# Kernel tuning notes

Measured on AMD Instinct MI355X. Metric: run time of the kernel, lower is better.

The kernel has to match this reference:

```python
import jax, jax.numpy as jnp
import numpy as np
from jax import lax

D = 512
K = 5
HID = 2 * D
EPS = 1e-5


def layernorm(x, g, b):
    mu = jnp.mean(x, axis=-1, keepdims=True)
    var = jnp.mean((x - mu) ** 2, axis=-1, keepdims=True)
    return (x - mu) * lax.rsqrt(var + EPS) * g + b


def setup_inputs() -> dict:
    key = jax.random.key(0)
    ks = jax.random.split(key, 16)
    B, T = 8, 4096
    sc = lambda fan: 1.0 / np.sqrt(fan)
    return {
        "x": jax.random.normal(ks[0], (B, T, D), jnp.float32),
        "decay_logit": jnp.zeros((D,), jnp.float32),
        "W_out": jax.random.uniform(ks[1], (D, D), jnp.float32, -sc(D), sc(D)),
        "b_out": jax.random.uniform(ks[2], (D,), jnp.float32, -sc(D), sc(D)),
        "conv_w": jax.random.uniform(ks[3], (D, 1, K), jnp.float32, -sc(K), sc(K)),
        "conv_b": jax.random.uniform(ks[4], (D,), jnp.float32, -sc(K), sc(K)),
        "ln1_g": jnp.ones((D,), jnp.float32),
        "ln1_b": jnp.zeros((D,), jnp.float32),
        "ln2_g": jnp.ones((D,), jnp.float32),
        "ln2_b": jnp.zeros((D,), jnp.float32),
        "W1": jax.random.uniform(ks[5], (HID, D), jnp.float32, -sc(D), sc(D)),
        "b1": jax.random.uniform(ks[6], (HID,), jnp.float32, -sc(D), sc(D)),
        "W2": jax.random.uniform(ks[7], (D, HID), jnp.float32, -sc(HID), sc(HID)),
        "b2": jax.random.uniform(ks[8], (D,), jnp.float32, -sc(HID), sc(HID)),
    }


def retention_core(xn, decay_logit, W_out, b_out, conv_w, conv_b):
    # xn: [B, T, D]
    B, T, _ = xn.shape
    a = jax.nn.sigmoid(decay_logit)  # [D]

    def step(s, xt):  # s, xt: [B, D]
        s = a * s + (1.0 - a) * xt
        return s, s

    s0 = jnp.zeros((B, D), xn.dtype)
    _, ss = lax.scan(step, s0, jnp.swapaxes(xn, 0, 1))  # [T, B, D]
    ss = jnp.swapaxes(ss, 0, 1)  # [B, T, D]
    y_ret = jnp.einsum("btd,ed->bte", ss, W_out) + b_out

    # depthwise conv1d, 'same' padding (K odd)
    xc = jnp.swapaxes(xn, 1, 2)  # [B, D, T]
    pad = (K - 1) // 2
    y_loc = lax.conv_general_dilated(
        xc, conv_w, window_strides=(1,), padding=[(pad, pad)],
        feature_group_count=D, dimension_numbers=("NCH", "OIH", "NCH"))
    y_loc = jnp.swapaxes(y_loc + conv_b[None, :, None], 1, 2)  # [B, T, D]
    return y_ret + y_loc


def reference(x, decay_logit, W_out, b_out, conv_w, conv_b,
              ln1_g, ln1_b, ln2_g, ln2_b, W1, b1, W2, b2):
    y = retention_core(layernorm(x, ln1_g, ln1_b),
                       decay_logit, W_out, b_out, conv_w, conv_b)
    x = x + y
    h = layernorm(x, ln2_g, ln2_b)
    h = jax.nn.gelu(jnp.einsum("btd,hd->bth", h, W1) + b1, approximate=False)
    y = jnp.einsum("bth,dh->btd", h, W2) + b2
    return x + y
```

## Files before the change

kernel.cpp:

```cpp
#include <hip/hip_runtime.h>
#include <stdint.h>

typedef unsigned short u16;

#define DIM 512
#define HIDN 1024
#define TT 4096
#define BB 8
#define MM 32768
#define CH 128
#define CL 32

__device__ __forceinline__ u16 f2bf(float f) {
  union { float f; uint32_t u; } v; v.f = f;
  uint32_t u = v.u;
  uint32_t r = u + 0x7fffu + ((u >> 16) & 1u);
  return (u16)(r >> 16);
}
__device__ __forceinline__ float bf2f(u16 h) {
  union { uint32_t u; float f; } v; v.u = ((uint32_t)h) << 16; return v.f;
}

typedef __bf16 bf16x8 __attribute__((ext_vector_type(8)));
typedef float f32x4 __attribute__((ext_vector_type(4)));

__global__ __launch_bounds__(256) void prep_kernel(
    const float* __restrict__ wout, const float* __restrict__ w1,
    const float* __restrict__ w2, const float* __restrict__ dl,
    const float* __restrict__ convw,
    u16* __restrict__ wout_h, u16* __restrict__ w1_h, u16* __restrict__ w2_h,
    float* __restrict__ a, float* __restrict__ oma, float* __restrict__ aL,
    float* __restrict__ convwT) {
  int i = blockIdx.x * 256 + threadIdx.x;
  if (i < DIM * DIM) wout_h[i] = f2bf(wout[i]);
  if (i < HIDN * DIM) { w1_h[i] = f2bf(w1[i]); w2_h[i] = f2bf(w2[i]); }
  if (i < 5 * DIM) {
    int kk = i / DIM, n = i - kk * DIM;
    convwT[i] = convw[n * 5 + kk];
  }
  if (i < DIM) {
    float av = 1.0f / (1.0f + expf(-dl[i]));
    a[i] = av; oma[i] = 1.0f - av; aL[i] = powf(av, (float)CL);
  }
}

__global__ __launch_bounds__(256) void ln_rows(
    const float* __restrict__ xin, const float* __restrict__ g,
    const float* __restrict__ bvec, u16* __restrict__ out) {
  int lane = threadIdx.x & 63, wave = threadIdx.x >> 6;
  size_t row = (size_t)blockIdx.x * 4 + wave;
  const float4* xr = (const float4*)(xin + row * DIM);
  float4 v0 = xr[lane * 2 + 0];
  float4 v1 = xr[lane * 2 + 1];
  float s1 = v0.x + v0.y + v0.z + v0.w + v1.x + v1.y + v1.z + v1.w;
  float s2 = v0.x * v0.x + v0.y * v0.y + v0.z * v0.z + v0.w * v0.w
           + v1.x * v1.x + v1.y * v1.y + v1.z * v1.z + v1.w * v1.w;
#pragma unroll
  for (int o = 1; o < 64; o <<= 1) { s1 += __shfl_xor(s1, o); s2 += __shfl_xor(s2, o); }
  float mu = s1 * (1.0f / DIM);
  float var = s2 * (1.0f / DIM) - mu * mu;
  float rs = rsqrtf(var + 1e-5f);
  const float4* gr = (const float4*)g;
  const float4* br = (const float4*)bvec;
  float4 g0 = gr[lane * 2], g1 = gr[lane * 2 + 1];
  float4 b0 = br[lane * 2], b1 = br[lane * 2 + 1];
  uint32_t p0 = (uint32_t)f2bf((v0.x - mu) * rs * g0.x + b0.x) | ((uint32_t)f2bf((v0.y - mu) * rs * g0.y + b0.y) << 16);
  uint32_t p1 = (uint32_t)f2bf((v0.z - mu) * rs * g0.z + b0.z) | ((uint32_t)f2bf((v0.w - mu) * rs * g0.w + b0.w) << 16);
  uint32_t p2 = (uint32_t)f2bf((v1.x - mu) * rs * g1.x + b1.x) | ((uint32_t)f2bf((v1.y - mu) * rs * g1.y + b1.y) << 16);
  uint32_t p3 = (uint32_t)f2bf((v1.z - mu) * rs * g1.z + b1.z) | ((uint32_t)f2bf((v1.w - mu) * rs * g1.w + b1.w) << 16);
  uint4 pk; pk.x = p0; pk.y = p1; pk.z = p2; pk.w = p3;
  ((uint4*)(out + row * DIM))[lane] = pk;
}

__global__ __launch_bounds__(256) void scan_local(
    const u16* __restrict__ xn, const float* __restrict__ a,
    const float* __restrict__ oma, float* __restrict__ carry) {
  int idx = blockIdx.x * 256 + threadIdx.x;
  int dp = (idx & 255) * 2;
  int c = (idx >> 8) & (CH - 1);
  int b = idx >> 15;
  float a0 = a[dp], a1 = a[dp + 1], o0 = oma[dp], o1 = oma[dp + 1];
  const uint32_t* xp = (const uint32_t*)(xn + ((size_t)(b * TT + c * CL)) * DIM + dp);
  float s0 = 0.f, s1 = 0.f;
#pragma unroll
  for (int i = 0; i < CL; ++i) {
    uint32_t u = xp[(size_t)i * (DIM / 2)];
    s0 = fmaf(a0, s0, o0 * bf2f((u16)(u & 0xffffu)));
    s1 = fmaf(a1, s1, o1 * bf2f((u16)(u >> 16)));
  }
  float2 cv; cv.x = s0; cv.y = s1;
  *(float2*)&carry[((size_t)(b * CH + c)) * DIM + dp] = cv;
}

__global__ __launch_bounds__(256) void scan_carry(
    const float* __restrict__ carry, const float* __restrict__ aL,
    float* __restrict__ start) {
  int idx = blockIdx.x * 256 + threadIdx.x;
  int d = idx & (DIM - 1);
  int b = idx >> 9;
  float al = aL[d];
  float s = 0.f;
#pragma unroll 8
  for (int c = 0; c < CH; ++c) {
    size_t o = ((size_t)(b * CH + c)) * DIM + d;
    start[o] = s;
    s = fmaf(al, s, carry[o]);
  }
}

__global__ __launch_bounds__(256) void scan_emit(
    const u16* __restrict__ xn, const float* __restrict__ a,
    const float* __restrict__ oma, const float* __restrict__ start,
    u16* __restrict__ ss) {
  int idx = blockIdx.x * 256 + threadIdx.x;
  int dp = (idx & 255) * 2;
  int c = (idx >> 8) & (CH - 1);
  int b = idx >> 15;
  float a0 = a[dp], a1 = a[dp + 1], o0 = oma[dp], o1 = oma[dp + 1];
  const uint32_t* xp = (const uint32_t*)(xn + ((size_t)(b * TT + c * CL)) * DIM + dp);
  uint32_t* sp = (uint32_t*)(ss + ((size_t)(b * TT + c * CL)) * DIM + dp);
  float2 st = *(const float2*)&start[((size_t)(b * CH + c)) * DIM + dp];
  float s0 = st.x, s1 = st.y;
#pragma unroll
  for (int i = 0; i < CL; ++i) {
    uint32_t u = xp[(size_t)i * (DIM / 2)];
    s0 = fmaf(a0, s0, o0 * bf2f((u16)(u & 0xffffu)));
    s1 = fmaf(a1, s1, o1 * bf2f((u16)(u >> 16)));
    sp[(size_t)i * (DIM / 2)] = (uint32_t)f2bf(s0) | ((uint32_t)f2bf(s1) << 16);
  }
}

template <int Kd, int NCOL, int EPI>
__global__ __launch_bounds__(256) void gemm_bt(
    const u16* __restrict__ A, const u16* __restrict__ Bmat,
    const float* __restrict__ bias, const float* __restrict__ resid,
    const u16* __restrict__ xn, const float* __restrict__ convwT,
    const float* __restrict__ convb, float* __restrict__ outf,
    u16* __restrict__ outh) {
  __shared__ alignas(16) u16 sA[2][128 * 64];
  __shared__ alignas(16) u16 sB[2][128 * 64];
  const int tid = threadIdx.x;
  const int lane = tid & 63, wave = tid >> 6;
  const int wr = (wave >> 1) * 64, wc = (wave & 1) * 64;
  const int rA = lane & 15, q = lane >> 4;

  const int lin = blockIdx.x;
  const int tile_col = (lin >> 3) & (NCOL - 1);
  const int tile_row = (lin & 7) + 8 * ((lin >> 3) / NCOL);
  const size_t rowTile = (size_t)tile_row * 128;
  const size_t colTile = (size_t)tile_col * 128;

  f32x4 acc[4][4];
#pragma unroll
  for (int i = 0; i < 4; i++)
#pragma unroll
    for (int j = 0; j < 4; j++) acc[i][j] = (f32x4){0.f, 0.f, 0.f, 0.f};

  const u16* Abase = A + rowTile * Kd;
  const u16* Bbase = Bmat + colTile * Kd;

  const int lrow = lane >> 3;
  const int lslot = lane & 7;
  const int gk = ((lslot ^ lrow) & 7) * 8;

  auto stage = [&](int kt, int buf) {
#pragma unroll
    for (int it = 0; it < 4; ++it) {
      const int m0 = (it * 4 + wave) * 8;
      const u16* ga = Abase + (size_t)(m0 + lrow) * Kd + kt + gk;
      const u16* gb = Bbase + (size_t)(m0 + lrow) * Kd + kt + gk;
      __builtin_amdgcn_global_load_lds(
          (const __attribute__((address_space(1))) void*)ga,
          (__attribute__((address_space(3))) void*)&sA[buf][m0 * 64], 16, 0, 0);
      __builtin_amdgcn_global_load_lds(
          (const __attribute__((address_space(1))) void*)gb,
          (__attribute__((address_space(3))) void*)&sB[buf][m0 * 64], 16, 0, 0);
    }
  };

  constexpr int NI = Kd / 64;
  stage(0, 0);
#pragma unroll 1
  for (int i = 0; i < NI; ++i) {
    __asm__ __volatile__("s_barrier" ::: "memory");
    if (i + 1 < NI) {
      stage((i + 1) * 64, (i + 1) & 1);
      __asm__ __volatile__("s_waitcnt vmcnt(8)" ::: "memory");
    } else {
      __asm__ __volatile__("s_waitcnt vmcnt(0)" ::: "memory");
    }
    __asm__ __volatile__("s_barrier" ::: "memory");
    const u16* bufA = sA[i & 1];
    const u16* bufB = sB[i & 1];
#pragma unroll
    for (int ks = 0; ks < 2; ++ks) {
      bf16x8 af[4], bfr[4];
#pragma unroll
      for (int mi = 0; mi < 4; ++mi) {
        int r = wr + mi * 16 + rA;
        int pos = ((ks * 4 + q) ^ (r & 7));
        af[mi] = *(const bf16x8*)&bufA[r * 64 + pos * 8];
      }
#pragma unroll
      for (int ni = 0; ni < 4; ++ni) {
        int r = wc + ni * 16 + rA;
        int pos = ((ks * 4 + q) ^ (r & 7));
        bfr[ni] = *(const bf16x8*)&bufB[r * 64 + pos * 8];
      }
#pragma unroll
      for (int mi = 0; mi < 4; ++mi)
#pragma unroll
        for (int ni = 0; ni < 4; ++ni)
          acc[mi][ni] = __builtin_amdgcn_mfma_f32_16x16x32_bf16(bfr[ni], af[mi], acc[mi][ni], 0, 0, 0);
    }
  }

#pragma unroll
  for (int mi = 0; mi < 4; ++mi) {
    size_t m = rowTile + wr + mi * 16 + rA;
#pragma unroll
    for (int ni = 0; ni < 4; ++ni) {
      int n0 = (int)colTile + wc + ni * 16 + q * 4;
      f32x4 v = acc[mi][ni];
      float4 bv = *(const float4*)&bias[n0];
      float val0 = v[0] + bv.x, val1 = v[1] + bv.y, val2 = v[2] + bv.z, val3 = v[3] + bv.w;
      if constexpr (EPI == 0) {
        int t = (int)(m & (TT - 1));
        float4 cb = *(const float4*)&convb[n0];
        float4 rv = *(const float4*)&resid[m * DIM + n0];
        val0 += cb.x + rv.x; val1 += cb.y + rv.y; val2 += cb.z + rv.z; val3 += cb.w + rv.w;
#pragma unroll
        for (int kk = 0; kk < 5; ++kk) {
          int ttc = t + kk - 2;
          if (ttc >= 0 && ttc < TT) {
            uint2 xv = *(const uint2*)&xn[(m + (size_t)kk - 2) * DIM + n0];
            float4 wv = *(const float4*)&convwT[kk * DIM + n0];
            val0 = fmaf(wv.x, bf2f((u16)(xv.x & 0xffffu)), val0);
            val1 = fmaf(wv.y, bf2f((u16)(xv.x >> 16)), val1);
            val2 = fmaf(wv.z, bf2f((u16)(xv.y & 0xffffu)), val2);
            val3 = fmaf(wv.w, bf2f((u16)(xv.y >> 16)), val3);
          }
        }
        float4 ov; ov.x = val0; ov.y = val1; ov.z = val2; ov.w = val3;
        *(float4*)&outf[m * DIM + n0] = ov;
      } else if constexpr (EPI == 1) {
        const float isq2 = 0.70710678118654752f;
        float g0 = 0.5f * val0 * (1.0f + erff(val0 * isq2));
        float g1 = 0.5f * val1 * (1.0f + erff(val1 * isq2));
        float g2 = 0.5f * val2 * (1.0f + erff(val2 * isq2));
        float g3 = 0.5f * val3 * (1.0f + erff(val3 * isq2));
        uint2 pk;
        pk.x = (uint32_t)f2bf(g0) | ((uint32_t)f2bf(g1) << 16);
        pk.y = (uint32_t)f2bf(g2) | ((uint32_t)f2bf(g3) << 16);
        *(uint2*)&outh[m * HIDN + n0] = pk;
      } else {
        float4 rv = *(const float4*)&resid[m * DIM + n0];
        float4 ov;
        ov.x = val0 + rv.x; ov.y = val1 + rv.y; ov.z = val2 + rv.z; ov.w = val3 + rv.w;
        *(float4*)&outf[m * DIM + n0] = ov;
      }
    }
  }
}

extern "C" void kernel_launch(void* const* d_in, const int* in_sizes, int n_in,
                              void* d_out, int out_size, void* d_ws, size_t ws_size,
                              hipStream_t stream) {
  const float* x      = (const float*)d_in[0];
  const float* dl     = (const float*)d_in[1];
  const float* W_out  = (const float*)d_in[2];
  const float* b_out  = (const float*)d_in[3];
  const float* conv_w = (const float*)d_in[4];
  const float* conv_b = (const float*)d_in[5];
  const float* ln1_g  = (const float*)d_in[6];
  const float* ln1_b  = (const float*)d_in[7];
  const float* ln2_g  = (const float*)d_in[8];
  const float* ln2_b  = (const float*)d_in[9];
  const float* W1     = (const float*)d_in[10];
  const float* b1     = (const float*)d_in[11];
  const float* W2     = (const float*)d_in[12];
  const float* b2     = (const float*)d_in[13];

  char* ws = (char*)d_ws;
  u16*   wout_h = (u16*)(ws + 0);
  u16*   w1_h   = (u16*)(ws + 524288);
  u16*   w2_h   = (u16*)(ws + 1572864);
  float* a_buf  = (float*)(ws + 2621440);
  float* oma    = (float*)(ws + 2623488);
  float* aL     = (float*)(ws + 2625536);
  float* convwT = (float*)(ws + 2627584);
  float* carry  = (float*)(ws + (4u << 20));
  float* start  = (float*)(ws + 6291456);
  u16*   xn  = (u16*)(ws + (8u << 20));
  u16*   ssb = (u16*)(ws + (40u << 20));
  float* x1  = (float*)(ws + (72u << 20));
  u16*   h   = (u16*)(ws + (136u << 20));
  u16*   hg  = (u16*)(ws + (168u << 20));

  float* out = (float*)d_out;

  prep_kernel<<<2048, 256, 0, stream>>>(W_out, W1, W2, dl, conv_w, wout_h, w1_h, w2_h, a_buf, oma, aL, convwT);
  ln_rows<<<MM / 4, 256, 0, stream>>>(x, ln1_g, ln1_b, xn);
  scan_local<<<(BB * CH * DIM / 2) / 256, 256, 0, stream>>>(xn, a_buf, oma, carry);
  scan_carry<<<(BB * DIM) / 256, 256, 0, stream>>>(carry, aL, start);
  scan_emit<<<(BB * CH * DIM / 2) / 256, 256, 0, stream>>>(xn, a_buf, oma, start, ssb);
  gemm_bt<512, 4, 0><<<1024, 256, 0, stream>>>(ssb, wout_h, b_out, x, xn, convwT, conv_b, x1, nullptr);
  ln_rows<<<MM / 4, 256, 0, stream>>>(x1, ln2_g, ln2_b, h);
  gemm_bt<512, 8, 1><<<2048, 256, 0, stream>>>(h, w1_h, b1, nullptr, nullptr, nullptr, nullptr, nullptr, hg);
  gemm_bt<1024, 4, 2><<<1024, 256, 0, stream>>>(hg, w2_h, b2, x1, nullptr, nullptr, nullptr, out, nullptr);
}
```

Measured before the change: 389.4 us.

## Enlarge GEMM tiles to 256x256 with 8 waves and deeper LDS pipeline

Rewrites the bf16 GEMM to compute 256x256 output tiles per 512-thread block, using 128 KB of dynamic LDS. It double-buffers K-slices with a prefetch two stages ahead and splits the MFMA work into phases with s_setprio and barriers, so global-to-LDS loads overlap compute. The aim is more data reuse per LDS byte and fewer blocks. The trade-offs are higher register pressure (an 8x4 accumulator array) with possible spills, and only one block per CU, which leaves little latency hiding beyond the explicit pipeline.

```diff
diff --git a/kernel.cpp b/kernel.cpp
--- a/kernel.cpp
+++ b/kernel.cpp
@@ -131,107 +131,144 @@
 }
 
 template <int Kd, int NCOL, int EPI>
-__global__ __launch_bounds__(256) void gemm_bt(
+__global__ __launch_bounds__(512, 2) void gemm_bt(
     const u16* __restrict__ A, const u16* __restrict__ Bmat,
     const float* __restrict__ bias, const float* __restrict__ resid,
     const u16* __restrict__ xn, const float* __restrict__ convwT,
     const float* __restrict__ convb, float* __restrict__ outf,
     u16* __restrict__ outh) {
-  __shared__ alignas(16) u16 sA[2][128 * 64];
-  __shared__ alignas(16) u16 sB[2][128 * 64];
+  extern __shared__ __align__(16) u16 lds[];
+  u16* sAb = lds;
+  u16* sBb = lds + 32768;
   const int tid = threadIdx.x;
   const int lane = tid & 63, wave = tid >> 6;
-  const int wr = (wave >> 1) * 64, wc = (wave & 1) * 64;
+  const int wm = wave >> 2;
+  const int wn = wave & 3;
   const int rA = lane & 15, q = lane >> 4;
+  const int lrow = lane >> 3;
+  const int lslot = lane & 7;
+  const int gk = ((lslot ^ lrow) & 7) * 8;
 
   const int lin = blockIdx.x;
   const int tile_col = (lin >> 3) & (NCOL - 1);
   const int tile_row = (lin & 7) + 8 * ((lin >> 3) / NCOL);
-  const size_t rowTile = (size_t)tile_row * 128;
-  const size_t colTile = (size_t)tile_col * 128;
-
-  f32x4 acc[4][4];
-#pragma unroll
-  for (int i = 0; i < 4; i++)
-#pragma unroll
-    for (int j = 0; j < 4; j++) acc[i][j] = (f32x4){0.f, 0.f, 0.f, 0.f};
+  const size_t rowTile = (size_t)tile_row * 256;
+  const size_t colTile = (size_t)tile_col * 256;
 
   const u16* Abase = A + rowTile * Kd;
   const u16* Bbase = Bmat + colTile * Kd;
 
-  const int lrow = lane >> 3;
-  const int lslot = lane & 7;
-  const int gk = ((lslot ^ lrow) & 7) * 8;
+  f32x4 acc[8][4];
+#pragma unroll
+  for (int i = 0; i < 8; i++)
+#pragma unroll
+    for (int j = 0; j < 4; j++) acc[i][j] = (f32x4){0.f, 0.f, 0.f, 0.f};
 
   auto stage = [&](int kt, int buf) {
 #pragma unroll
-    for (int it = 0; it < 4; ++it) {
-      const int m0 = (it * 4 + wave) * 8;
-      const u16* ga = Abase + (size_t)(m0 + lrow) * Kd + kt + gk;
-      const u16* gb = Bbase + (size_t)(m0 + lrow) * Kd + kt + gk;
+    for (int j = 0; j < 4; ++j) {
+      const int g = j * 8 + wave;
+      const u16* ga = Abase + (size_t)(g * 8 + lrow) * Kd + kt + gk;
+      const u16* gb = Bbase + (size_t)(g * 8 + lrow) * Kd + kt + gk;
       __builtin_amdgcn_global_load_lds(
           (const __attribute__((address_space(1))) void*)ga,
-          (__attribute__((address_space(3))) void*)&sA[buf][m0 * 64], 16, 0, 0);
+          (__attribute__((address_space(3))) void*)(sAb + buf * 16384 + g * 512), 16, 0, 0);
       __builtin_amdgcn_global_load_lds(
           (const __attribute__((address_space(1))) void*)gb,
-          (__attribute__((address_space(3))) void*)&sB[buf][m0 * 64], 16, 0, 0);
+          (__attribute__((address_space(3))) void*)(sBb + buf * 16384 + g * 512), 16, 0, 0);
     }
   };
 
-  constexpr int NI = Kd / 64;
+  constexpr int NT = Kd / 64;
   stage(0, 0);
+  stage(64, 1);
+  __asm__ __volatile__("s_waitcnt vmcnt(8)" ::: "memory");
+  __asm__ __volatile__("s_barrier" ::: "memory");
+
+  const int sw = rA & 7;
 #pragma unroll 1
-  for (int i = 0; i < NI; ++i) {
-    __asm__ __volatile__("s_barrier" ::: "memory");
-    if (i + 1 < NI) {
-      stage((i + 1) * 64, (i + 1) & 1);
+  for (int t = 0; t < NT; ++t) {
+    const int p = t & 1;
+    const u16* bufA = sAb + p * 16384 + (wm * 128 + rA) * 64;
+    const u16* bufB = sBb + p * 16384 + (wn * 64 + rA) * 64;
+    bf16x8 afr[8][2], bfr[4][2];
+
+#pragma unroll
+    for (int ni = 0; ni < 4; ++ni)
+#pragma unroll
+      for (int ks = 0; ks < 2; ++ks)
+        bfr[ni][ks] = *(const bf16x8*)&bufB[ni * 1024 + (((ks * 4 + q) ^ sw) * 8)];
+#pragma unroll
+    for (int mi = 0; mi < 2; ++mi)
+#pragma unroll
+      for (int ks = 0; ks < 2; ++ks)
+        afr[mi][ks] = *(const bf16x8*)&bufA[mi * 1024 + (((ks * 4 + q) ^ sw) * 8)];
+    __asm__ __volatile__("s_barrier" ::: "memory");
+    __asm__ __volatile__("s_waitcnt lgkmcnt(0)" ::: "memory");
+    __builtin_amdgcn_s_setprio(1);
+#pragma unroll
+    for (int mi = 0; mi < 2; ++mi)
+#pragma unroll
+      for (int ni = 0; ni < 4; ++ni)
+#pragma unroll
+        for (int ks = 0; ks < 2; ++ks)
+          acc[mi][ni] = __builtin_amdgcn_mfma_f32_16x16x32_bf16(bfr[ni][ks], afr[mi][ks], acc[mi][ni], 0, 0, 0);
+    __builtin_amdgcn_s_setprio(0);
+    __asm__ __volatile__("s_barrier" ::: "memory");
+
+#pragma unroll
+    for (int mi = 2; mi < 8; ++mi)
+#pragma unroll
+      for (int ks = 0; ks < 2; ++ks)
+        afr[mi][ks] = *(const bf16x8*)&bufA[mi * 1024 + (((ks * 4 + q) ^ sw) * 8)];
+    __asm__ __volatile__("s_barrier" ::: "memory");
+    __asm__ __volatile__("s_waitcnt lgkmcnt(0)" ::: "memory");
+    __builtin_amdgcn_s_setprio(1);
+#pragma unroll
+    for (int mi = 2; mi < 4; ++mi)
+#pragma unroll
+      for (int ni = 0; ni < 4; ++ni)
+#pragma unroll
+        for (int ks = 0; ks < 2; ++ks)
+          acc[mi][ni] = __builtin_amdgcn_mfma_f32_16x16x32_bf16(bfr[ni][ks], afr[mi][ks], acc[mi][ni], 0, 0, 0);
+    __builtin_amdgcn_s_setprio(0);
+    __asm__ __volatile__("s_barrier" ::: "memory");
+
+    if (t + 2 < NT) stage((t + 2) * 64, p);
+    __builtin_amdgcn_s_setprio(1);
+#pragma unroll
+    for (int mi = 4; mi < 8; ++mi)
+#pragma unroll
+      for (int ni = 0; ni < 4; ++ni)
+#pragma unroll
+        for (int ks = 0; ks < 2; ++ks)
+          acc[mi][ni] = __builtin_amdgcn_mfma_f32_16x16x32_bf16(bfr[ni][ks], afr[mi][ks], acc[mi][ni], 0, 0, 0);
+    __builtin_amdgcn_s_setprio(0);
+    if (t + 2 < NT) {
       __asm__ __volatile__("s_waitcnt vmcnt(8)" ::: "memory");
-    } else {
+    } else if (t + 1 < NT) {
       __asm__ __volatile__("s_waitcnt vmcnt(0)" ::: "memory");
     }
     __asm__ __volatile__("s_barrier" ::: "memory");
-    const u16* bufA = sA[i & 1];
-    const u16* bufB = sB[i & 1];
-#pragma unroll
-    for (int ks = 0; ks < 2; ++ks) {
-      bf16x8 af[4], bfr[4];
-#pragma unroll
-      for (int mi = 0; mi < 4; ++mi) {
-        int r = wr + mi * 16 + rA;
-        int pos = ((ks * 4 + q) ^ (r & 7));
-        af[mi] = *(const bf16x8*)&bufA[r * 64 + pos * 8];
-      }
-#pragma unroll
-      for (int ni = 0; ni < 4; ++ni) {
-        int r = wc + ni * 16 + rA;
-        int pos = ((ks * 4 + q) ^ (r & 7));
-        bfr[ni] = *(const bf16x8*)&bufB[r * 64 + pos * 8];
-      }
-#pragma unroll
-      for (int mi = 0; mi < 4; ++mi)
-#pragma unroll
-        for (int ni = 0; ni < 4; ++ni)
-          acc[mi][ni] = __builtin_amdgcn_mfma_f32_16x16x32_bf16(bfr[ni], af[mi], acc[mi][ni], 0, 0, 0);
-    }
-  }
-
-#pragma unroll
-  for (int mi = 0; mi < 4; ++mi) {
-    size_t m = rowTile + wr + mi * 16 + rA;
+  }
+
+#pragma unroll
+  for (int mi = 0; mi < 8; ++mi) {
+    size_t m = rowTile + wm * 128 + mi * 16 + rA;
 #pragma unroll
     for (int ni = 0; ni < 4; ++ni) {
-      int n0 = (int)colTile + wc + ni * 16 + q * 4;
+      int n0 = (int)colTile + wn * 64 + ni * 16 + q * 4;
       f32x4 v = acc[mi][ni];
       float4 bv = *(const float4*)&bias[n0];
       float val0 = v[0] + bv.x, val1 = v[1] + bv.y, val2 = v[2] + bv.z, val3 = v[3] + bv.w;
       if constexpr (EPI == 0) {
-        int t = (int)(m & (TT - 1));
+        int tt = (int)(m & (TT - 1));
         float4 cb = *(const float4*)&convb[n0];
         float4 rv = *(const float4*)&resid[m * DIM + n0];
         val0 += cb.x + rv.x; val1 += cb.y + rv.y; val2 += cb.z + rv.z; val3 += cb.w + rv.w;
 #pragma unroll
         for (int kk = 0; kk < 5; ++kk) {
-          int ttc = t + kk - 2;
+          int ttc = tt + kk - 2;
           if (ttc >= 0 && ttc < TT) {
             uint2 xv = *(const uint2*)&xn[(m + (size_t)kk - 2) * DIM + n0];
             float4 wv = *(const float4*)&convwT[kk * DIM + n0];
@@ -299,13 +336,20 @@
 
   float* out = (float*)d_out;
 
+  hipFuncSetAttribute(reinterpret_cast<const void*>(&gemm_bt<512, 2, 0>),
+                      hipFuncAttributeMaxDynamicSharedMemorySize, 131072);
+  hipFuncSetAttribute(reinterpret_cast<const void*>(&gemm_bt<512, 4, 1>),
+                      hipFuncAttributeMaxDynamicSharedMemorySize, 131072);
+  hipFuncSetAttribute(reinterpret_cast<const void*>(&gemm_bt<1024, 2, 2>),
+                      hipFuncAttributeMaxDynamicSharedMemorySize, 131072);
+
   prep_kernel<<<2048, 256, 0, stream>>>(W_out, W1, W2, dl, conv_w, wout_h, w1_h, w2_h, a_buf, oma, aL, convwT);
   ln_rows<<<MM / 4, 256, 0, stream>>>(x, ln1_g, ln1_b, xn);
   scan_local<<<(BB * CH * DIM / 2) / 256, 256, 0, stream>>>(xn, a_buf, oma, carry);
   scan_carry<<<(BB * DIM) / 256, 256, 0, stream>>>(carry, aL, start);
   scan_emit<<<(BB * CH * DIM / 2) / 256, 256, 0, stream>>>(xn, a_buf, oma, start, ssb);
-  gemm_bt<512, 4, 0><<<1024, 256, 0, stream>>>(ssb, wout_h, b_out, x, xn, convwT, conv_b, x1, nullptr);
+  gemm_bt<512, 2, 0><<<256, 512, 131072, stream>>>(ssb, wout_h, b_out, x, xn, convwT, conv_b, x1, nullptr);
   ln_rows<<<MM / 4, 256, 0, stream>>>(x1, ln2_g, ln2_b, h);
-  gemm_bt<512, 8, 1><<<2048, 256, 0, stream>>>(h, w1_h, b1, nullptr, nullptr, nullptr, nullptr, nullptr, hg);
-  gemm_bt<1024, 4, 2><<<1024, 256, 0, stream>>>(hg, w2_h, b2, x1, nullptr, nullptr, nullptr, out, nullptr);
-}
+  gemm_bt<512, 4, 1><<<512, 512, 131072, stream>>>(h, w1_h, b1, nullptr, nullptr, nullptr, nullptr, nullptr, hg);
+  gemm_bt<1024, 2, 2><<<256, 512, 131072, stream>>>(hg, w2_h, b2, x1, nullptr, nullptr, nullptr, out, nullptr);
+}
```

New measurement: 401.8 us. +3.2%, slower.
